# Kernel tuning notes

Measured on AMD Instinct MI355X. Metric: run time of the kernel, lower is better.

## Reference

```python
import jax, jax.numpy as jnp
import numpy as np

SQRT2 = 1.4142135623730951
TARGET_DENSITY = 0.9
XL, YL, XH, YH = 0.0, 0.0, 1024.0, 1024.0
BSX, BSY = 2.0, 2.0
NM, NT, NF = 1_000_000, 10_000, 200_000
N_TOTAL = NM + NT + NF
NBX = int(round((XH - XL) / BSX))  # 512
NBY = int(round((YH - YL) / BSY))  # 512
K_MOV = 5   # ceil((max movable size 3 + 2*sqrt2*bs) / bs) with bs=2
K_FIX = 10  # ceil((max fixed size 16 + bs) / bs) with margin; extra bins overlap 0
PADDING = 1


def _splat(x, y, sx, sy, w, K):
    """Scatter-add exact rectangle/bin overlaps of each cell into a flat [NBX*NBY] map.
    x,y: lower-left corners [N]; sx,sy: sizes [N]; w: per-cell weight (ratio) [N]."""
    bx0 = jnp.floor((x - XL) / BSX).astype(jnp.int32)  # first impacted bin in x
    by0 = jnp.floor((y - YL) / BSY).astype(jnp.int32)
    ks = jnp.arange(K, dtype=jnp.int32)
    bx = bx0[:, None] + ks  # [N,K]
    by = by0[:, None] + ks
    ox = jnp.minimum(x[:, None] + sx[:, None], XL + (bx + 1) * BSX) - \
         jnp.maximum(x[:, None], XL + bx * BSX)
    oy = jnp.minimum(y[:, None] + sy[:, None], YL + (by + 1) * BSY) - \
         jnp.maximum(y[:, None], YL + by * BSY)
    ox = jnp.where((bx >= 0) & (bx < NBX), jnp.clip(ox, 0.0), 0.0)
    oy = jnp.where((by >= 0) & (by < NBY), jnp.clip(oy, 0.0), 0.0)
    bxc = jnp.clip(bx, 0, NBX - 1)
    byc = jnp.clip(by, 0, NBY - 1)
    v = w[:, None, None] * ox[:, :, None] * oy[:, None, :]        # [N,K,K]
    idx = (bxc[:, :, None] * NBY + byc[:, None, :]).reshape(-1)   # [N*K*K]
    return jnp.zeros(NBX * NBY, dtype=x.dtype).at[idx].add(v.reshape(-1))


def setup_inputs() -> dict:
    key = jax.random.key(0)
    k1, k2, k3, k4, k5, k6, k7, k8 = jax.random.split(key, 8)
    # node sizes: movable standard cells, fixed terminals (larger), fillers
    sx = jnp.concatenate([
        jax.random.uniform(k1, (NM,), minval=1.0, maxval=3.0),
        jax.random.uniform(k2, (NT,), minval=4.0, maxval=16.0),
        jax.random.uniform(k3, (NF,), minval=1.5, maxval=2.5)])
    sy = jnp.concatenate([
        jax.random.uniform(k4, (NM,), minval=1.0, maxval=3.0),
        jax.random.uniform(k5, (NT,), minval=4.0, maxval=16.0),
        jax.random.uniform(k6, (NF,), minval=1.5, maxval=2.5)])
    pos_x = jax.random.uniform(k7, (N_TOTAL,), minval=XL, maxval=XH - 16.0)
    pos_y = jax.random.uniform(k8, (N_TOTAL,), minval=YL, maxval=YH - 16.0)
    pos = jnp.concatenate([pos_x, pos_y])  # x coords then y coords
    return {"pos": pos, "node_size_x": sx, "node_size_y": sy}


def reference(pos, node_size_x, node_size_y):
    x = pos[:N_TOTAL]
    y = pos[N_TOTAL:]
    # --- initial density map from fixed terminals (exact overlap, no stretching) ---
    tsl = slice(NM, NM + NT)
    init_map = _splat(x[tsl], y[tsl], node_size_x[tsl], node_size_y[tsl],
                      jnp.ones((NT,), pos.dtype), K_FIX) * TARGET_DENSITY
    # --- movable + filler: stretch to >= bin_size*sqrt2, splat rescaled area ---
    sxc = jnp.maximum(node_size_x, BSX * SQRT2)
    syc = jnp.maximum(node_size_y, BSY * SQRT2)
    off_x = (node_size_x - sxc) * 0.5
    off_y = (node_size_y - syc) * 0.5
    ratio = (node_size_x * node_size_y) / (sxc * syc)
    mf = np.concatenate([np.arange(NM), np.arange(N_TOTAL - NF, N_TOTAL)])  # movable + filler
    dmap = init_map + _splat((x + off_x)[mf], (y + off_y)[mf], sxc[mf], syc[mf],
                             ratio[mf], K_MOV)
    dmap = dmap.reshape(NBX, NBY)
    # padding mask: border bins forced to target capacity
    bin_area = BSX * BSY
    ix = jnp.arange(NBX)
    iy = jnp.arange(NBY)
    pad = ((ix < PADDING) | (ix >= NBX - PADDING))[:, None] | \
          ((iy < PADDING) | (iy >= NBY - PADDING))[None, :]
    dmap = jnp.where(pad, TARGET_DENSITY * bin_area, dmap)
    density_cost = jnp.clip(dmap - TARGET_DENSITY * bin_area, 0.0).sum()[None]
    max_density = (dmap.max() / bin_area)[None]
    return density_cost, max_density
```

## Files before the change

### kernel.cpp

```cpp
#include <hip/hip_runtime.h>

#define NM_ 1000000
#define NT_ 10000
#define NF_ 200000
#define N_TOTAL_ 1210000
#define NBX_ 512
#define NBY_ 512
#define NBINS_ (NBX_ * NBY_)
#define TD_ 0.9f
#define PAD_VAL_ 3.6f
#define SQRT2x2_ 2.8284271247461903f

#define TSZ_ 16
#define TSH_ 4
#define TGX_ 32
#define NTILES_ 1024
#define HALO_ 2
#define TW_ 18
#define TAREA_ (TW_ * TW_)
#define CAPM_ 1536
#define CAPT_ 128
#define NB_ 512
#define NTH_ 512
#define CHUNK_ 2364

static __device__ __forceinline__ int imin_(int a, int b) { return a < b ? a : b; }
static __device__ __forceinline__ int imax_(int a, int b) { return a > b ? a : b; }

static __device__ __forceinline__ void fadd_(float* p, float v) {
    unsafeAtomicAdd(p, v);
}

__global__ __launch_bounds__(NTH_) void count_kernel(
        const float* __restrict__ px, const float* __restrict__ py,
        const float* __restrict__ sxp, const float* __restrict__ syp,
        int* __restrict__ cnt, int* __restrict__ cntT) {
    __shared__ int hist[NTILES_];
    for (int t = threadIdx.x; t < NTILES_; t += blockDim.x) hist[t] = 0;
    if (blockIdx.x == 0)
        for (int t = threadIdx.x; t < NTILES_; t += blockDim.x) cntT[t] = 0;
    __syncthreads();
    int b = blockIdx.x;
    int lo = b * CHUNK_, hi = imin_(lo + CHUNK_, N_TOTAL_);
    for (int i = lo + threadIdx.x; i < hi; i += blockDim.x) {
        if (i >= NM_ && i < NM_ + NT_) continue;
        float sx0 = sxp[i], sy0 = syp[i];
        float sxc = fmaxf(sx0, SQRT2x2_);
        float syc = fmaxf(sy0, SQRT2x2_);
        float x = px[i] + (sx0 - sxc) * 0.5f;
        float y = py[i] + (sy0 - syc) * 0.5f;
        int bx0 = (int)floorf(x * 0.5f);
        int by0 = (int)floorf(y * 0.5f);
        int t = (imax_(bx0, 0) >> TSH_) * TGX_ + (imax_(by0, 0) >> TSH_);
        atomicAdd(&hist[t], 1);
    }
    __syncthreads();
    for (int t = threadIdx.x; t < NTILES_; t += blockDim.x)
        cnt[t * NB_ + b] = hist[t];
}

__global__ void scan_kernel(int* __restrict__ cnt, int* __restrict__ totM,
                            float* __restrict__ out) {
    int tile = blockIdx.x * 4 + (threadIdx.x >> 6);
    int l = threadIdx.x & 63;
    int X = l & 7;
    int mrow = l >> 3;
    int* row = cnt + (size_t)tile * NB_;
    int c[8];
#pragma unroll
    for (int g = 0; g < 8; g++) c[g] = row[l + 64 * g];
    int off[8];
    int W = 0;
#pragma unroll
    for (int g = 0; g < 8; g++) {
        int v = c[g];
#pragma unroll
        for (int s = 1; s < 8; s <<= 1) {
            int n = __shfl_up(v, 8 * s);
            if (mrow >= s) v += n;
        }
        off[g] = W + v - c[g];
        W += __shfl(v, X + 56);
    }
    int B = 0, tot = 0;
#pragma unroll
    for (int Xp = 0; Xp < 8; Xp++) {
        int t = __shfl(W, Xp);
        if (Xp < X) B += t;
        tot += t;
    }
#pragma unroll
    for (int g = 0; g < 8; g++) row[l + 64 * g] = B + off[g];
    if (l == 0) totM[tile] = tot;
    if (blockIdx.x == 0 && threadIdx.x == 0) { out[0] = 0.0f; out[1] = 0.0f; }
}

__global__ __launch_bounds__(NTH_) void scatter_kernel(
        const float* __restrict__ px, const float* __restrict__ py,
        const float* __restrict__ sxp, const float* __restrict__ syp,
        const int* __restrict__ start, int* __restrict__ cntT,
        float4* __restrict__ recM, float4* __restrict__ recT) {
    __shared__ int cur[NTILES_];
    int b = blockIdx.x;
    for (int t = threadIdx.x; t < NTILES_; t += blockDim.x)
        cur[t] = start[t * NB_ + b];
    __syncthreads();
    int lo = b * CHUNK_, hi = imin_(lo + CHUNK_, N_TOTAL_);
    for (int i = lo + threadIdx.x; i < hi; i += blockDim.x) {
        float sx0 = sxp[i], sy0 = syp[i];
        bool fix = (i >= NM_) && (i < NM_ + NT_);
        if (!fix) {
            float sxc = fmaxf(sx0, SQRT2x2_);
            float syc = fmaxf(sy0, SQRT2x2_);
            float x = px[i] + (sx0 - sxc) * 0.5f;
            float y = py[i] + (sy0 - syc) * 0.5f;
            int bx0 = (int)floorf(x * 0.5f);
            int by0 = (int)floorf(y * 0.5f);
            int t = (imax_(bx0, 0) >> TSH_) * TGX_ + (imax_(by0, 0) >> TSH_);
            int slot = atomicAdd(&cur[t], 1);
            if (slot < CAPM_) recM[(size_t)t * CAPM_ + slot] = make_float4(x, y, sx0, sy0);
        } else {
            float x = px[i], y = py[i];
            int bx0 = (int)floorf(x * 0.5f);
            int by0 = (int)floorf(y * 0.5f);
            int bxm = imin_((int)floorf((x + sx0) * 0.5f), NBX_ - 1);
            int bym = imin_((int)floorf((y + sy0) * 0.5f), NBY_ - 1);
            int txA = bx0 >> TSH_, txB = bxm >> TSH_;
            int tyA = by0 >> TSH_, tyB = bym >> TSH_;
            for (int tx = txA; tx <= txB; tx++)
                for (int ty = tyA; ty <= tyB; ty++) {
                    int t = tx * TGX_ + ty;
                    int slot = atomicAdd(&cntT[t], 1);
                    if (slot < CAPT_) recT[(size_t)t * CAPT_ + slot] = make_float4(x, y, sx0, sy0);
                }
        }
    }
}

__global__ __launch_bounds__(512) void accumS_kernel(
        const float4* __restrict__ recM, const float4* __restrict__ recT,
        const int* __restrict__ totM, const int* __restrict__ cntT,
        float* __restrict__ tiles) {
    __shared__ float4 srec[CAPM_];
    __shared__ float  sw[CAPM_];
    __shared__ float  m[TAREA_];
    __shared__ int    boff[257];
    __shared__ int    bcur[256];
    int tile = blockIdx.x;
    int tx16 = (tile >> 5) << TSH_;
    int ty16 = (tile & (TGX_ - 1)) << TSH_;
    for (int k = threadIdx.x; k < TAREA_; k += 512) m[k] = 0.0f;
    if (threadIdx.x < 256) bcur[threadIdx.x] = 0;
    __syncthreads();
    int nM = imin_(totM[tile], CAPM_);
    const float4* rM = recM + (size_t)tile * CAPM_;
    for (int i = threadIdx.x; i < nM; i += 512) {
        float4 r = rM[i];
        int kr = imin_(imax_((int)floorf(r.x * 0.5f) - tx16, 0), 15);
        int kc = imin_(imax_((int)floorf(r.y * 0.5f) - ty16, 0), 15);
        atomicAdd(&bcur[kr * 16 + kc], 1);
    }
    __syncthreads();
    if (threadIdx.x < 64) {
        int l = threadIdx.x;
        int c0 = bcur[4 * l], c1 = bcur[4 * l + 1], c2 = bcur[4 * l + 2], c3 = bcur[4 * l + 3];
        int s = c0 + c1 + c2 + c3;
        int incl = s;
#pragma unroll
        for (int off = 1; off < 64; off <<= 1) {
            int n = __shfl_up(incl, off);
            if (l >= off) incl += n;
        }
        int run = incl - s;
        boff[4 * l] = run;
        boff[4 * l + 1] = run + c0;
        boff[4 * l + 2] = run + c0 + c1;
        boff[4 * l + 3] = run + c0 + c1 + c2;
        if (l == 63) boff[256] = incl;
    }
    __syncthreads();
    if (threadIdx.x < 256) bcur[threadIdx.x] = boff[threadIdx.x];
    __syncthreads();
    for (int i = threadIdx.x; i < nM; i += 512) {
        float4 r = rM[i];
        float sxc = fmaxf(r.z, SQRT2x2_);
        float syc = fmaxf(r.w, SQRT2x2_);
        float w = (r.z * r.w) / (sxc * syc);
        int kr = imin_(imax_((int)floorf(r.x * 0.5f) - tx16, 0), 15);
        int kc = imin_(imax_((int)floorf(r.y * 0.5f) - ty16, 0), 15);
        int slot = atomicAdd(&bcur[kr * 16 + kc], 1);
        srec[slot] = make_float4(r.x, r.y, r.x + sxc, r.y + syc);
        sw[slot] = w;
    }
    int nT = imin_(cntT[tile], CAPT_);
    const float4* rT = recT + (size_t)tile * CAPT_;
    for (int i = threadIdx.x; i < nT; i += 512) {
        float4 r = rT[i];
        float xe = r.x + r.z, ye = r.y + r.w;
        int bx0 = (int)floorf(r.x * 0.5f);
        int by0 = (int)floorf(r.y * 0.5f);
        int bxA = imax_(bx0, tx16), byA = imax_(by0, ty16);
        int bxB = imin_(imin_((int)floorf(xe * 0.5f), tx16 + TSZ_ - 1), NBX_ - 1);
        int byB = imin_(imin_((int)floorf(ye * 0.5f), ty16 + TSZ_ - 1), NBY_ - 1);
        for (int bx = bxA; bx <= bxB; bx++) {
            float ox = fminf(xe, (bx + 1) * 2.0f) - fmaxf(r.x, bx * 2.0f);
            ox = fmaxf(ox, 0.0f) * TD_;
            for (int by = byA; by <= byB; by++) {
                float oy = fminf(ye, (by + 1) * 2.0f) - fmaxf(r.y, by * 2.0f);
                atomicAdd(&m[(bx - tx16) * TW_ + (by - ty16)], ox * fmaxf(oy, 0.0f));
            }
        }
    }
    __syncthreads();
    if (threadIdx.x < TAREA_) {
        int r = threadIdx.x / TW_;
        int c = threadIdx.x % TW_;
        float blx = (tx16 + r) * 2.0f, bhx = blx + 2.0f;
        float bly = (ty16 + c) * 2.0f, bhy = bly + 2.0f;
        int krA = imax_(r - 2, 0), krB = imin_(r, 15);
        int kcA = imax_(c - 2, 0), kcB = imin_(c, 15);
        float acc = 0.0f;
        for (int kr = krA; kr <= krB; kr++) {
            int j0 = boff[kr * 16 + kcA];
            int j1 = boff[kr * 16 + kcB + 1];
            for (int j = j0; j < j1; j++) {
                float4 t = srec[j];
                float ox = fminf(t.z, bhx) - fmaxf(t.x, blx);
                float oy = fminf(t.w, bhy) - fmaxf(t.y, bly);
                acc = fmaf(sw[j], fmaxf(ox, 0.0f) * fmaxf(oy, 0.0f), acc);
            }
        }
        m[threadIdx.x] += acc;
    }
    __syncthreads();
    for (int k = threadIdx.x; k < TAREA_; k += 512)
        tiles[(size_t)tile * TAREA_ + k] = m[k];
}

__global__ void reduce2_kernel(const float* __restrict__ tiles, float* __restrict__ out) {
    float sum = 0.0f, mx = 0.0f;
    for (int i = blockIdx.x * blockDim.x + threadIdx.x; i < NBINS_;
         i += gridDim.x * blockDim.x) {
        int gx = i >> 9, gy = i & (NBY_ - 1);
        float v;
        bool pad = (gx < 1) | (gx >= NBX_ - 1) | (gy < 1) | (gy >= NBY_ - 1);
        if (pad) {
            v = PAD_VAL_;
        } else {
            int tx = gx >> TSH_, lx = gx & (TSZ_ - 1);
            int ty = gy >> TSH_, ly = gy & (TSZ_ - 1);
            v = tiles[(size_t)(tx * TGX_ + ty) * TAREA_ + lx * TW_ + ly];
            if (lx < HALO_ && tx > 0)
                v += tiles[(size_t)((tx - 1) * TGX_ + ty) * TAREA_ + (lx + TSZ_) * TW_ + ly];
            if (ly < HALO_ && ty > 0)
                v += tiles[(size_t)(tx * TGX_ + (ty - 1)) * TAREA_ + lx * TW_ + (ly + TSZ_)];
            if (lx < HALO_ && ly < HALO_ && tx > 0 && ty > 0)
                v += tiles[(size_t)((tx - 1) * TGX_ + (ty - 1)) * TAREA_ + (lx + TSZ_) * TW_ + (ly + TSZ_)];
        }
        sum += fmaxf(v - PAD_VAL_, 0.0f);
        mx = fmaxf(mx, v);
    }
#pragma unroll
    for (int off = 32; off > 0; off >>= 1) {
        sum += __shfl_down(sum, off);
        mx = fmaxf(mx, __shfl_down(mx, off));
    }
    __shared__ float ssum[8], smx[8];
    int lane = threadIdx.x & 63, wid = threadIdx.x >> 6;
    if (lane == 0) { ssum[wid] = sum; smx[wid] = mx; }
    __syncthreads();
    if (threadIdx.x == 0) {
        int nw = blockDim.x >> 6;
        float s = 0.0f, m = 0.0f;
        for (int w = 0; w < nw; w++) { s += ssum[w]; m = fmaxf(m, smx[w]); }
        fadd_(&out[0], s);
        atomicMax((unsigned int*)&out[1], __float_as_uint(m * 0.25f));
    }
}

__global__ void zero_kernel(float* __restrict__ dmap, float* __restrict__ out) {
    int i = blockIdx.x * blockDim.x + threadIdx.x;
    if (i < NBINS_) dmap[i] = 0.0f;
    if (i == 0) { out[0] = 0.0f; out[1] = 0.0f; }
}

__global__ void splat_fix(const float* __restrict__ px, const float* __restrict__ py,
                          const float* __restrict__ sxp, const float* __restrict__ syp,
                          float* __restrict__ dmap) {
    int t = blockIdx.x * blockDim.x + threadIdx.x;
    if (t >= NT_) return;
    int i = NM_ + t;
    float x = px[i], y = py[i], sx = sxp[i], sy = syp[i];
    int bx0 = (int)floorf(x * 0.5f), by0 = (int)floorf(y * 0.5f);
    for (int kx = 0; kx < 10; kx++) {
        int bx = bx0 + kx;
        if (bx < 0 || bx >= NBX_) continue;
        float ox = fminf(x + sx, (bx + 1) * 2.0f) - fmaxf(x, bx * 2.0f);
        if (ox <= 0.0f) continue;
        for (int ky = 0; ky < 10; ky++) {
            int by = by0 + ky;
            if (by < 0 || by >= NBY_) continue;
            float oy = fminf(y + sy, (by + 1) * 2.0f) - fmaxf(y, by * 2.0f);
            if (oy <= 0.0f) continue;
            fadd_(&dmap[bx * NBY_ + by], TD_ * ox * oy);
        }
    }
}

__global__ void splat_mov(const float* __restrict__ px, const float* __restrict__ py,
                          const float* __restrict__ sxp, const float* __restrict__ syp,
                          float* __restrict__ dmap) {
    int i = blockIdx.x * blockDim.x + threadIdx.x;
    if (i >= N_TOTAL_) return;
    if (i >= NM_ && i < NM_ + NT_) return;
    float sx = sxp[i], sy = syp[i];
    float sxc = fmaxf(sx, SQRT2x2_), syc = fmaxf(sy, SQRT2x2_);
    float x = px[i] + (sx - sxc) * 0.5f, y = py[i] + (sy - syc) * 0.5f;
    float w = (sx * sy) / (sxc * syc);
    int bx0 = (int)floorf(x * 0.5f), by0 = (int)floorf(y * 0.5f);
    for (int kx = 0; kx < 5; kx++) {
        int bx = bx0 + kx;
        if (bx < 0 || bx >= NBX_) continue;
        float ox = fminf(x + sxc, (bx + 1) * 2.0f) - fmaxf(x, bx * 2.0f);
        if (ox <= 0.0f) continue;
        for (int ky = 0; ky < 5; ky++) {
            int by = by0 + ky;
            if (by < 0 || by >= NBY_) continue;
            float oy = fminf(y + syc, (by + 1) * 2.0f) - fmaxf(y, by * 2.0f);
            if (oy <= 0.0f) continue;
            fadd_(&dmap[bx * NBY_ + by], w * ox * oy);
        }
    }
}

__global__ void reduce_kernel(const float* __restrict__ dmap, float* __restrict__ out) {
    float sum = 0.0f, mx = 0.0f;
    for (int i = blockIdx.x * blockDim.x + threadIdx.x; i < NBINS_;
         i += gridDim.x * blockDim.x) {
        int ix = i >> 9, iy = i & (NBY_ - 1);
        float v = dmap[i];
        bool pad = (ix < 1) | (ix >= NBX_ - 1) | (iy < 1) | (iy >= NBY_ - 1);
        if (pad) v = PAD_VAL_;
        sum += fmaxf(v - PAD_VAL_, 0.0f);
        mx = fmaxf(mx, v);
    }
#pragma unroll
    for (int off = 32; off > 0; off >>= 1) {
        sum += __shfl_down(sum, off);
        mx = fmaxf(mx, __shfl_down(mx, off));
    }
    __shared__ float ssum[8], smx[8];
    int lane = threadIdx.x & 63, wid = threadIdx.x >> 6;
    if (lane == 0) { ssum[wid] = sum; smx[wid] = mx; }
    __syncthreads();
    if (threadIdx.x == 0) {
        int nw = blockDim.x >> 6;
        float s = 0.0f, m = 0.0f;
        for (int w = 0; w < nw; w++) { s += ssum[w]; m = fmaxf(m, smx[w]); }
        fadd_(&out[0], s);
        atomicMax((unsigned int*)&out[1], __float_as_uint(m * 0.25f));
    }
}

extern "C" void kernel_launch(void* const* d_in, const int* in_sizes, int n_in,
                              void* d_out, int out_size, void* d_ws, size_t ws_size,
                              hipStream_t stream) {
    const float* pos = (const float*)d_in[0];
    const float* nsx = (const float*)d_in[1];
    const float* nsy = (const float*)d_in[2];
    const float* px = pos;
    const float* py = pos + N_TOTAL_;
    float* out = (float*)d_out;

    size_t o_cnt   = 0;
    size_t o_totM  = o_cnt + (size_t)NB_ * NTILES_ * 4;
    size_t o_cntT  = o_totM + (size_t)NTILES_ * 4;
    size_t o_recM  = o_cntT + (size_t)NTILES_ * 4;
    size_t o_recT  = o_recM + (size_t)NTILES_ * CAPM_ * 16;
    size_t o_tiles = o_recT + (size_t)NTILES_ * CAPT_ * 16;
    size_t req     = o_tiles + (size_t)NTILES_ * TAREA_ * 4;

    if (ws_size >= req) {
        char* ws = (char*)d_ws;
        int*    cnt   = (int*)(ws + o_cnt);
        int*    totM  = (int*)(ws + o_totM);
        int*    cntT  = (int*)(ws + o_cntT);
        float4* recM  = (float4*)(ws + o_recM);
        float4* recT  = (float4*)(ws + o_recT);
        float*  tiles = (float*)(ws + o_tiles);

        count_kernel<<<NB_, NTH_, 0, stream>>>(px, py, nsx, nsy, cnt, cntT);
        scan_kernel<<<NTILES_ / 4, 256, 0, stream>>>(cnt, totM, out);
        scatter_kernel<<<NB_, NTH_, 0, stream>>>(px, py, nsx, nsy, cnt, cntT, recM, recT);
        accumS_kernel<<<NTILES_, 512, 0, stream>>>(recM, recT, totM, cntT, tiles);
        reduce2_kernel<<<1024, 256, 0, stream>>>(tiles, out);
    } else {
        float* dmap = (float*)d_ws;
        zero_kernel<<<(NBINS_ + 255) / 256, 256, 0, stream>>>(dmap, out);
        splat_fix<<<(NT_ + 255) / 256, 256, 0, stream>>>(px, py, nsx, nsy, dmap);
        splat_mov<<<(N_TOTAL_ + 255) / 256, 256, 0, stream>>>(px, py, nsx, nsy, dmap);
        reduce_kernel<<<1024, 256, 0, stream>>>(dmap, out);
    }
}
```

Measured before the change: 91.15 us.

## Quantize movable cell records to 16-bit fixed point and precompute bin keys

Movable-cell records written by the scatter pass are now stored as ushort4, holding tile-relative positions and sizes quantized at 1/1024, instead of float4. A separate byte key per record carries the in-tile bin index so the accumulation kernel no longer recomputes it. The count matrix is also transposed so that count and scatter kernels write and read contiguously per block. The aim is to halve the record traffic between scatter and accumulate and remove redundant arithmetic, at the cost of quantization error in positions and sizes and strided reads in the scan kernel.

Measured after the change: 91.40 us. Within noise of the previous version (+0.3%).

```diff
diff --git a/kernel.cpp b/kernel.cpp
--- a/kernel.cpp
+++ b/kernel.cpp
@@ -23,6 +23,9 @@
 #define NB_ 512
 #define NTH_ 512
 #define CHUNK_ 2364
+#define NGRP_ 8
+#define QS_ 1024.0f
+#define IQS_ (1.0f / 1024.0f)
 
 static __device__ __forceinline__ int imin_(int a, int b) { return a < b ? a : b; }
 static __device__ __forceinline__ int imax_(int a, int b) { return a > b ? a : b; }
@@ -56,7 +59,7 @@
     }
     __syncthreads();
     for (int t = threadIdx.x; t < NTILES_; t += blockDim.x)
-        cnt[t * NB_ + b] = hist[t];
+        cnt[b * NTILES_ + t] = hist[t];
 }
 
 __global__ void scan_kernel(int* __restrict__ cnt, int* __restrict__ totM,
@@ -65,14 +68,13 @@
     int l = threadIdx.x & 63;
     int X = l & 7;
     int mrow = l >> 3;
-    int* row = cnt + (size_t)tile * NB_;
-    int c[8];
-#pragma unroll
-    for (int g = 0; g < 8; g++) c[g] = row[l + 64 * g];
-    int off[8];
+    int c[NGRP_];
+#pragma unroll
+    for (int g = 0; g < NGRP_; g++) c[g] = cnt[(l + 64 * g) * NTILES_ + tile];
+    int off[NGRP_];
     int W = 0;
 #pragma unroll
-    for (int g = 0; g < 8; g++) {
+    for (int g = 0; g < NGRP_; g++) {
         int v = c[g];
 #pragma unroll
         for (int s = 1; s < 8; s <<= 1) {
@@ -90,7 +92,7 @@
         tot += t;
     }
 #pragma unroll
-    for (int g = 0; g < 8; g++) row[l + 64 * g] = B + off[g];
+    for (int g = 0; g < NGRP_; g++) cnt[(l + 64 * g) * NTILES_ + tile] = B + off[g];
     if (l == 0) totM[tile] = tot;
     if (blockIdx.x == 0 && threadIdx.x == 0) { out[0] = 0.0f; out[1] = 0.0f; }
 }
@@ -99,11 +101,12 @@
         const float* __restrict__ px, const float* __restrict__ py,
         const float* __restrict__ sxp, const float* __restrict__ syp,
         const int* __restrict__ start, int* __restrict__ cntT,
-        float4* __restrict__ recM, float4* __restrict__ recT) {
+        ushort4* __restrict__ recM, unsigned char* __restrict__ keyM,
+        float4* __restrict__ recT) {
     __shared__ int cur[NTILES_];
     int b = blockIdx.x;
     for (int t = threadIdx.x; t < NTILES_; t += blockDim.x)
-        cur[t] = start[t * NB_ + b];
+        cur[t] = start[b * NTILES_ + t];
     __syncthreads();
     int lo = b * CHUNK_, hi = imin_(lo + CHUNK_, N_TOTAL_);
     for (int i = lo + threadIdx.x; i < hi; i += blockDim.x) {
@@ -116,9 +119,23 @@
             float y = py[i] + (sy0 - syc) * 0.5f;
             int bx0 = (int)floorf(x * 0.5f);
             int by0 = (int)floorf(y * 0.5f);
-            int t = (imax_(bx0, 0) >> TSH_) * TGX_ + (imax_(by0, 0) >> TSH_);
+            int txo = (imax_(bx0, 0) >> TSH_) << TSH_;
+            int tyo = (imax_(by0, 0) >> TSH_) << TSH_;
+            int t = (txo >> TSH_) * TGX_ + (tyo >> TSH_);
             int slot = atomicAdd(&cur[t], 1);
-            if (slot < CAPM_) recM[(size_t)t * CAPM_ + slot] = make_float4(x, y, sx0, sy0);
+            if (slot < CAPM_) {
+                float bxo = txo * 2.0f - 16.0f;
+                float byo = tyo * 2.0f - 16.0f;
+                ushort4 q;
+                q.x = (unsigned short)__float2int_rn((x - bxo) * QS_);
+                q.y = (unsigned short)__float2int_rn((y - byo) * QS_);
+                q.z = (unsigned short)__float2int_rn(sx0 * QS_);
+                q.w = (unsigned short)__float2int_rn(sy0 * QS_);
+                recM[(size_t)t * CAPM_ + slot] = q;
+                int kr = imin_(imax_(bx0 - txo, 0), 15);
+                int kc = imin_(imax_(by0 - tyo, 0), 15);
+                keyM[(size_t)t * CAPM_ + slot] = (unsigned char)(kr * 16 + kc);
+            }
         } else {
             float x = px[i], y = py[i];
             int bx0 = (int)floorf(x * 0.5f);
@@ -138,7 +155,8 @@
 }
 
 __global__ __launch_bounds__(512) void accumS_kernel(
-        const float4* __restrict__ recM, const float4* __restrict__ recT,
+        const ushort4* __restrict__ recM, const unsigned char* __restrict__ keyM,
+        const float4* __restrict__ recT,
         const int* __restrict__ totM, const int* __restrict__ cntT,
         float* __restrict__ tiles) {
     __shared__ float4 srec[CAPM_];
@@ -153,13 +171,10 @@
     if (threadIdx.x < 256) bcur[threadIdx.x] = 0;
     __syncthreads();
     int nM = imin_(totM[tile], CAPM_);
-    const float4* rM = recM + (size_t)tile * CAPM_;
-    for (int i = threadIdx.x; i < nM; i += 512) {
-        float4 r = rM[i];
-        int kr = imin_(imax_((int)floorf(r.x * 0.5f) - tx16, 0), 15);
-        int kc = imin_(imax_((int)floorf(r.y * 0.5f) - ty16, 0), 15);
-        atomicAdd(&bcur[kr * 16 + kc], 1);
-    }
+    const ushort4* rq = recM + (size_t)tile * CAPM_;
+    const unsigned char* kM = keyM + (size_t)tile * CAPM_;
+    for (int i = threadIdx.x; i < nM; i += 512)
+        atomicAdd(&bcur[kM[i]], 1);
     __syncthreads();
     if (threadIdx.x < 64) {
         int l = threadIdx.x;
@@ -181,15 +196,18 @@
     __syncthreads();
     if (threadIdx.x < 256) bcur[threadIdx.x] = boff[threadIdx.x];
     __syncthreads();
+    float bxo = tx16 * 2.0f - 16.0f;
+    float byo = ty16 * 2.0f - 16.0f;
     for (int i = threadIdx.x; i < nM; i += 512) {
-        float4 r = rM[i];
-        float sxc = fmaxf(r.z, SQRT2x2_);
-        float syc = fmaxf(r.w, SQRT2x2_);
-        float w = (r.z * r.w) / (sxc * syc);
-        int kr = imin_(imax_((int)floorf(r.x * 0.5f) - tx16, 0), 15);
-        int kc = imin_(imax_((int)floorf(r.y * 0.5f) - ty16, 0), 15);
-        int slot = atomicAdd(&bcur[kr * 16 + kc], 1);
-        srec[slot] = make_float4(r.x, r.y, r.x + sxc, r.y + syc);
+        ushort4 q = rq[i];
+        float x = bxo + q.x * IQS_;
+        float y = byo + q.y * IQS_;
+        float sx0 = q.z * IQS_, sy0 = q.w * IQS_;
+        float sxc = fmaxf(sx0, SQRT2x2_);
+        float syc = fmaxf(sy0, SQRT2x2_);
+        float w = (sx0 * sy0) / (sxc * syc);
+        int slot = atomicAdd(&bcur[kM[i]], 1);
+        srec[slot] = make_float4(x, y, x + sxc, y + syc);
         sw[slot] = w;
     }
     int nT = imin_(cntT[tile], CAPT_);
@@ -376,23 +394,25 @@
     size_t o_totM  = o_cnt + (size_t)NB_ * NTILES_ * 4;
     size_t o_cntT  = o_totM + (size_t)NTILES_ * 4;
     size_t o_recM  = o_cntT + (size_t)NTILES_ * 4;
-    size_t o_recT  = o_recM + (size_t)NTILES_ * CAPM_ * 16;
+    size_t o_keyM  = o_recM + (size_t)NTILES_ * CAPM_ * 8;
+    size_t o_recT  = o_keyM + (size_t)NTILES_ * CAPM_;
     size_t o_tiles = o_recT + (size_t)NTILES_ * CAPT_ * 16;
     size_t req     = o_tiles + (size_t)NTILES_ * TAREA_ * 4;
 
     if (ws_size >= req) {
         char* ws = (char*)d_ws;
-        int*    cnt   = (int*)(ws + o_cnt);
-        int*    totM  = (int*)(ws + o_totM);
-        int*    cntT  = (int*)(ws + o_cntT);
-        float4* recM  = (float4*)(ws + o_recM);
-        float4* recT  = (float4*)(ws + o_recT);
-        float*  tiles = (float*)(ws + o_tiles);
+        int*           cnt   = (int*)(ws + o_cnt);
+        int*           totM  = (int*)(ws + o_totM);
+        int*           cntT  = (int*)(ws + o_cntT);
+        ushort4*       recM  = (ushort4*)(ws + o_recM);
+        unsigned char* keyM  = (unsigned char*)(ws + o_keyM);
+        float4*        recT  = (float4*)(ws + o_recT);
+        float*         tiles = (float*)(ws + o_tiles);
 
         count_kernel<<<NB_, NTH_, 0, stream>>>(px, py, nsx, nsy, cnt, cntT);
         scan_kernel<<<NTILES_ / 4, 256, 0, stream>>>(cnt, totM, out);
-        scatter_kernel<<<NB_, NTH_, 0, stream>>>(px, py, nsx, nsy, cnt, cntT, recM, recT);
-        accumS_kernel<<<NTILES_, 512, 0, stream>>>(recM, recT, totM, cntT, tiles);
+        scatter_kernel<<<NB_, NTH_, 0, stream>>>(px, py, nsx, nsy, cnt, cntT, recM, keyM, recT);
+        accumS_kernel<<<NTILES_, 512, 0, stream>>>(recM, keyM, recT, totM, cntT, tiles);
         reduce2_kernel<<<1024, 256, 0, stream>>>(tiles, out);
     } else {
         float* dmap = (float*)d_ws;
```
